# Performance work log

Hardware: AMD Instinct MI355X
Metric: run time of the kernel (lower is better)

## Reference

```python
import jax, jax.numpy as jnp
import numpy as np

B = 128
N_IN = 32      # n_inp_capsules
D_IN = 8       # dim_inp_capsules
N_OUT = 10     # n_out_capsules
D_OUT = 16     # dim_out_capsules
DIM = 12       # dim_input (spatial side)
N = N_IN * DIM * DIM  # 4608 total input capsule positions
NUM_ROUTING = 3


def setup_inputs() -> dict:
    key = jax.random.key(0)
    k1, k2 = jax.random.split(key)
    x = jax.random.normal(k1, (B, D_IN, N_IN, DIM, DIM), dtype=jnp.float32)
    weight = jax.random.normal(k2, (D_IN, D_OUT, N, N_OUT), dtype=jnp.float32)
    return {"x": x, "weight": weight}


def squash(s, axis):
    # s_sq/(1+s_sq) * s / sqrt(s_sq)  -- exactly the module's squash (no eps)
    s_sq = jnp.sum(s * s, axis=axis, keepdims=True)
    return s_sq / (1.0 + s_sq) * s / jnp.sqrt(s_sq)


def reference(x, weight):
    b_sz = x.shape[0]
    # view(B, C, -1).permute(0,2,1): (B, N, D_IN)
    u = x.reshape(b_sz, D_IN, -1).transpose(0, 2, 1)
    # u_hat[b,o,n,j] = sum_d u[b,n,d] * weight[d,o,n,j]  (replaces the double python loop)
    u_hat = jnp.einsum('bnd,donj->bonj', u, weight)  # (B, D_OUT, N, N_OUT)
    b = jnp.zeros((b_sz, 1, N, N_OUT), dtype=u_hat.dtype)
    s = None
    for _ in range(NUM_ROUTING):
        c = jax.nn.softmax(b, axis=3)                      # over output capsules
        s = squash(jnp.sum(u_hat * c, axis=2), axis=1)     # (B, D_OUT, N_OUT)
        b = b + jnp.sum(s[:, :, None, :] * u_hat, axis=1, keepdims=True)
    return s  # torch returns s.squeeze() of (B, D_OUT, 1, N_OUT) -> (B, D_OUT, N_OUT)
```

## Files before the change

kernel.cpp:

```cpp
#include <hip/hip_runtime.h>
#include <math.h>

#define NTOT 4608

typedef _Float16 f16;
typedef _Float16 f16x4 __attribute__((ext_vector_type(4)));
typedef _Float16 f16x8 __attribute__((ext_vector_type(8)));
typedef float f32x4 __attribute__((ext_vector_type(4)));

__global__ __launch_bounds__(256) void make_ut(const float* __restrict__ x, f16* __restrict__ ut) {
    const int t = blockIdx.x * 256 + threadIdx.x;
    const int b = t / NTOT, n = t - b * NTOT;
    f16x8 v;
    #pragma unroll
    for (int d = 0; d < 8; ++d)
        v[d] = (f16)x[((size_t)b * 8 + d) * NTOT + n];
    *reinterpret_cast<f16x8*>(ut + (size_t)t * 8) = v;
}

__global__ __launch_bounds__(320) void make_wt(const float* __restrict__ W, f16* __restrict__ wt) {
    __shared__ float l[2560];
    const int k = threadIdx.x;
    const int n0 = blockIdx.x * 2;
    #pragma unroll
    for (int r = 0; r < 8; ++r) {
        const int f = k + r * 320;
        const int p = f / 20, q = f - p * 20;
        l[f] = W[(size_t)p * 46080 + n0 * 10 + q];
    }
    __syncthreads();
    const int half = k / 160, rr = k - half * 160;
    const int j = rr >> 4, o = rr & 15;
    f16x8 v;
    #pragma unroll
    for (int d = 0; d < 8; ++d)
        v[d] = (f16)l[d * 320 + o * 20 + half * 10 + j];
    *reinterpret_cast<f16x8*>(wt + ((size_t)(n0 + half) * 160 + rr) * 8) = v;
}

__global__ __launch_bounds__(256) void kernelA(const f16* __restrict__ ut, const f16* __restrict__ wt,
                                               f16* __restrict__ uh, float* __restrict__ partial) {
    __shared__ float s0t[4][16][164];
    const int tid = threadIdx.x, w = tid >> 6, lane = tid & 63;
    const int col = lane & 15, qA = lane >> 4;
    const int chunk = blockIdx.x, bg = blockIdx.y, b0 = bg * 16;
    const int b = b0 + col;
    const int nstart = chunk * 32 + w * 8;

    const f16* ab = wt + ((size_t)nstart * 160 + col) * 8;
    const f16* ub = ut + ((size_t)b * NTOT + nstart) * 8;
    f16* uhw = uh + (size_t)nstart * 20480 + (size_t)(qA >> 1) * 1024 + b * 8 + (qA & 1) * 4;

    const f32x4 cz = {0.f, 0.f, 0.f, 0.f};
    f32x4 s0a[10];
    #pragma unroll
    for (int m = 0; m < 10; ++m) s0a[m] = cz;

    for (int nl = 0; nl < 8; ++nl) {
        const f16x8 bf = *reinterpret_cast<const f16x8*>(ub + nl * 8);
        #pragma unroll
        for (int m = 0; m < 10; ++m) {
            const f16x8 af = *reinterpret_cast<const f16x8*>(ab + ((size_t)nl * 160 + m * 16) * 8);
            f32x4 C = __builtin_amdgcn_mfma_f32_16x16x32_f16(af, bf, cz, 0, 0, 0);
            s0a[m] += C;
            f16x4 hv;
            hv[0] = (f16)(0.25f * C[0]); hv[1] = (f16)(0.25f * C[1]);
            hv[2] = (f16)(0.25f * C[2]); hv[3] = (f16)(0.25f * C[3]);
            *reinterpret_cast<f16x4*>(uhw + (size_t)nl * 20480 + m * 2048) = hv;
        }
    }

    #pragma unroll
    for (int m = 0; m < 10; ++m)
        *reinterpret_cast<f32x4*>(&s0t[w][col][m * 16 + qA * 4]) = s0a[m];
    __syncthreads();
    for (int r = tid; r < 2560; r += 256) {
        const int row = r / 160, slot = r - row * 160;
        float v = s0t[0][row][slot] + s0t[1][row][slot] + s0t[2][row][slot] + s0t[3][row][slot];
        partial[((size_t)chunk * 128 + b0 + row) * 160 + slot] = v;
    }
}

__global__ __launch_bounds__(256) void kernelB(const f16* __restrict__ uh, const float* __restrict__ Ar,
                                               float* __restrict__ partial) {
    __shared__ float s1t[4][16][164];
    const int tid = threadIdx.x, w = tid >> 6, lane = tid & 63;
    const int g = lane & 15, q = lane >> 4;
    const int chunk = blockIdx.x, bg = blockIdx.y;
    const int b = bg * 16 + g;
    const int nstart = chunk * 16 + w * 4;
    const bool qlow = (q < 2);

    float Af[5][8];
    #pragma unroll
    for (int s = 0; s < 5; ++s) {
        f32x4 a0 = *reinterpret_cast<const f32x4*>(Ar + (size_t)b * 160 + (4 * s + q) * 8);
        f32x4 a1 = *reinterpret_cast<const f32x4*>(Ar + (size_t)b * 160 + (4 * s + q) * 8 + 4);
        #pragma unroll
        for (int t = 0; t < 4; ++t) { Af[s][t] = a0[t]; Af[s][4 + t] = a1[t]; }
    }

    float P[5][8];
    #pragma unroll
    for (int s = 0; s < 5; ++s)
        #pragma unroll
        for (int t = 0; t < 8; ++t) P[s][t] = 0.f;

    const f16* uhb = uh + (size_t)nstart * 20480 + (size_t)q * 1024 + b * 8;

    for (int nl = 0; nl < 4; ++nl) {
        f16x8 U[5];
        #pragma unroll
        for (int s = 0; s < 5; ++s)
            U[s] = *reinterpret_cast<const f16x8*>(uhb + (size_t)nl * 20480 + s * 4096);

        float tp[5];
        #pragma unroll
        for (int s = 0; s < 5; ++s) {
            float acc = 0.f;
            #pragma unroll
            for (int t = 0; t < 8; ++t)
                acc = fmaf(Af[s][t], (float)U[s][t], acc);
            tp[s] = acc;
        }

        float tt[10];
        #pragma unroll
        for (int s = 0; s < 5; ++s) {
            float tq = tp[s] + __shfl_xor(tp[s], 16, 64);
            float tr = __shfl_xor(tq, 32, 64);
            tt[2 * s]     = qlow ? tq : tr;
            tt[2 * s + 1] = qlow ? tr : tq;
        }

        float mx = fmaxf(fmaxf(fmaxf(fmaxf(tt[0], tt[1]), fmaxf(tt[2], tt[3])),
                               fmaxf(fmaxf(tt[4], tt[5]), fmaxf(tt[6], tt[7]))),
                         fmaxf(tt[8], tt[9]));
        float c[10], sum = 0.f;
        #pragma unroll
        for (int j = 0; j < 10; ++j) { float e = __expf(tt[j] - mx); c[j] = e; sum += e; }
        const float inv = 1.0f / sum;

        #pragma unroll
        for (int s = 0; s < 5; ++s) {
            const float cm = (qlow ? c[2 * s] : c[2 * s + 1]) * inv;
            #pragma unroll
            for (int t = 0; t < 8; ++t)
                P[s][t] = fmaf(cm, (float)U[s][t], P[s][t]);
        }
    }

    #pragma unroll
    for (int s = 0; s < 5; ++s) {
        const int sg = 4 * s + q;
        f32x4 p0 = {P[s][0], P[s][1], P[s][2], P[s][3]};
        f32x4 p1 = {P[s][4], P[s][5], P[s][6], P[s][7]};
        *reinterpret_cast<f32x4*>(&s1t[w][g][sg * 8])     = p0;
        *reinterpret_cast<f32x4*>(&s1t[w][g][sg * 8 + 4]) = p1;
    }
    __syncthreads();
    for (int r = tid; r < 2560; r += 256) {
        const int row = r / 160, slot = r - row * 160;
        float v = s1t[0][row][slot] + s1t[1][row][slot] + s1t[2][row][slot] + s1t[3][row][slot];
        partial[((size_t)chunk * 128 + bg * 16 + row) * 160 + slot] = v;
    }
}

__global__ __launch_bounds__(160) void red1(const float* __restrict__ partial,
                                            float* __restrict__ p2, int nc8) {
    const int b = blockIdx.x, sl = blockIdx.y, k = threadIdx.x;
    const float* p = partial + ((size_t)sl * nc8 * 128 + b) * 160 + k;
    float acc = 0.f;
    for (int c = 0; c < nc8; ++c) acc += p[(size_t)c * 128 * 160];
    p2[((size_t)b * 8 + sl) * 160 + k] = acc;
}

template<int MODE>
__global__ __launch_bounds__(160) void phase2f(const float* __restrict__ p2,
                                               float* __restrict__ Ar, float* __restrict__ out,
                                               float sumscale) {
    const int b = blockIdx.x, k = threadIdx.x;
    __shared__ float srs[160];
    float acc = 0.f;
    #pragma unroll
    for (int sl = 0; sl < 8; ++sl) acc += p2[((size_t)b * 8 + sl) * 160 + k];
    acc *= sumscale;
    srs[k] = acc;
    __syncthreads();
    const int j = k >> 4;
    float ssq = 0.f;
    #pragma unroll
    for (int o = 0; o < 16; ++o) { float v = srs[j * 16 + o]; ssq = fmaf(v, v, ssq); }
    const float s = acc * ssq / ((1.f + ssq) * sqrtf(ssq));
    if (MODE == 0)      Ar[(size_t)b * 160 + k] = s;
    else if (MODE == 1) Ar[(size_t)b * 160 + k] += s;
    else { const int o = k & 15; out[(size_t)b * 160 + o * 10 + j] = s; }
}

extern "C" void kernel_launch(void* const* d_in, const int* in_sizes, int n_in,
                              void* d_out, int out_size, void* d_ws, size_t ws_size,
                              hipStream_t stream) {
    const float* x = (const float*)d_in[0];
    const float* W = (const float*)d_in[1];
    float* out = (float*)d_out;

    f16* ut = (f16*)d_ws;
    f16* wt = ut + (size_t)128 * NTOT * 8;
    f16* uh = wt + (size_t)NTOT * 160 * 8;
    float* Ar = (float*)(uh + (size_t)NTOT * 20 * 128 * 8);
    float* partial = Ar + 128 * 160;
    float* p2 = partial + (size_t)288 * 128 * 160;

    make_ut<<<2304, 256, 0, stream>>>(x, ut);
    make_wt<<<2304, 320, 0, stream>>>(W, wt);

    dim3 gA(144, 8), gB(288, 8), gR(128, 8);
    kernelA<<<gA, 256, 0, stream>>>(ut, wt, uh, partial);
    red1<<<gR, 160, 0, stream>>>(partial, p2, 144 / 8);
    phase2f<0><<<128, 160, 0, stream>>>(p2, Ar, out, 0.025f);

    kernelB<<<gB, 256, 0, stream>>>(uh, Ar, partial);
    red1<<<gR, 160, 0, stream>>>(partial, p2, 288 / 8);
    phase2f<1><<<128, 160, 0, stream>>>(p2, Ar, out, 1.0f);

    kernelB<<<gB, 256, 0, stream>>>(uh, Ar, partial);
    red1<<<gR, 160, 0, stream>>>(partial, p2, 288 / 8);
    phase2f<2><<<128, 160, 0, stream>>>(p2, Ar, out, 1.0f);
}
```

Measured before the change: 174.6 us.

## Fuse prep kernels, merge reduction with squash, and double kernelB work per block

Merges the two input-conversion kernels into one launch, with the block index choosing between weight transpose and input transpose. Replaces the two-stage red1+phase2f reduction with one 640-thread kernel per batch that sums partials and squashes. Makes each kernelB block cover 32 positions instead of 16, halving the partial count so it matches kernelA's layout. This cuts launch count and partial-buffer traffic, at the cost of fewer blocks in kernelB. It also adds a __syncthreads inside a branch whose condition splits a wavefront, which is risky.

```diff
diff --git a/kernel.cpp b/kernel.cpp
--- a/kernel.cpp
+++ b/kernel.cpp
@@ -8,34 +8,37 @@
 typedef _Float16 f16x8 __attribute__((ext_vector_type(8)));
 typedef float f32x4 __attribute__((ext_vector_type(4)));
 
-__global__ __launch_bounds__(256) void make_ut(const float* __restrict__ x, f16* __restrict__ ut) {
-    const int t = blockIdx.x * 256 + threadIdx.x;
-    const int b = t / NTOT, n = t - b * NTOT;
-    f16x8 v;
-    #pragma unroll
-    for (int d = 0; d < 8; ++d)
-        v[d] = (f16)x[((size_t)b * 8 + d) * NTOT + n];
-    *reinterpret_cast<f16x8*>(ut + (size_t)t * 8) = v;
-}
-
-__global__ __launch_bounds__(320) void make_wt(const float* __restrict__ W, f16* __restrict__ wt) {
+__global__ __launch_bounds__(320) void prep(const float* __restrict__ x, const float* __restrict__ W,
+                                            f16* __restrict__ ut, f16* __restrict__ wt) {
     __shared__ float l[2560];
     const int k = threadIdx.x;
-    const int n0 = blockIdx.x * 2;
-    #pragma unroll
-    for (int r = 0; r < 8; ++r) {
-        const int f = k + r * 320;
-        const int p = f / 20, q = f - p * 20;
-        l[f] = W[(size_t)p * 46080 + n0 * 10 + q];
-    }
-    __syncthreads();
-    const int half = k / 160, rr = k - half * 160;
-    const int j = rr >> 4, o = rr & 15;
-    f16x8 v;
-    #pragma unroll
-    for (int d = 0; d < 8; ++d)
-        v[d] = (f16)l[d * 320 + o * 20 + half * 10 + j];
-    *reinterpret_cast<f16x8*>(wt + ((size_t)(n0 + half) * 160 + rr) * 8) = v;
+    if (blockIdx.x < 2304) {
+        const int n0 = blockIdx.x * 2;
+        #pragma unroll
+        for (int r = 0; r < 8; ++r) {
+            const int f = k + r * 320;
+            const int p = f / 20, q = f - p * 20;
+            l[f] = W[(size_t)p * 46080 + n0 * 10 + q];
+        }
+        __syncthreads();
+        const int half = k / 160, rr = k - half * 160;
+        const int j = rr >> 4, o = rr & 15;
+        f16x8 v;
+        #pragma unroll
+        for (int d = 0; d < 8; ++d)
+            v[d] = (f16)l[d * 320 + o * 20 + half * 10 + j];
+        *reinterpret_cast<f16x8*>(wt + ((size_t)(n0 + half) * 160 + rr) * 8) = v;
+    } else {
+        const int t = (blockIdx.x - 2304) * 320 + k;
+        if (t < 128 * NTOT) {
+            const int b = t / NTOT, n = t - b * NTOT;
+            f16x8 v;
+            #pragma unroll
+            for (int d = 0; d < 8; ++d)
+                v[d] = (f16)x[((size_t)b * 8 + d) * NTOT + n];
+            *reinterpret_cast<f16x8*>(ut + (size_t)t * 8) = v;
+        }
+    }
 }
 
 __global__ __launch_bounds__(256) void kernelA(const f16* __restrict__ ut, const f16* __restrict__ wt,
@@ -88,7 +91,7 @@
     const int g = lane & 15, q = lane >> 4;
     const int chunk = blockIdx.x, bg = blockIdx.y;
     const int b = bg * 16 + g;
-    const int nstart = chunk * 16 + w * 4;
+    const int nstart = chunk * 32 + w * 8;
     const bool qlow = (q < 2);
 
     float Af[5][8];
@@ -108,7 +111,7 @@
 
     const f16* uhb = uh + (size_t)nstart * 20480 + (size_t)q * 1024 + b * 8;
 
-    for (int nl = 0; nl < 4; ++nl) {
+    for (int nl = 0; nl < 8; ++nl) {
         f16x8 U[5];
         #pragma unroll
         for (int s = 0; s < 5; ++s)
@@ -166,35 +169,34 @@
     }
 }
 
-__global__ __launch_bounds__(160) void red1(const float* __restrict__ partial,
-                                            float* __restrict__ p2, int nc8) {
-    const int b = blockIdx.x, sl = blockIdx.y, k = threadIdx.x;
-    const float* p = partial + ((size_t)sl * nc8 * 128 + b) * 160 + k;
+template<int MODE>
+__global__ __launch_bounds__(640) void reduce_squash(const float* __restrict__ partial,
+                                                     float* __restrict__ Ar, float* __restrict__ out,
+                                                     float sumscale) {
+    const int b = blockIdx.x;
+    const int k = threadIdx.x % 160;
+    const int r = threadIdx.x / 160;
+    __shared__ float red[4][160];
     float acc = 0.f;
-    for (int c = 0; c < nc8; ++c) acc += p[(size_t)c * 128 * 160];
-    p2[((size_t)b * 8 + sl) * 160 + k] = acc;
-}
-
-template<int MODE>
-__global__ __launch_bounds__(160) void phase2f(const float* __restrict__ p2,
-                                               float* __restrict__ Ar, float* __restrict__ out,
-                                               float sumscale) {
-    const int b = blockIdx.x, k = threadIdx.x;
-    __shared__ float srs[160];
-    float acc = 0.f;
-    #pragma unroll
-    for (int sl = 0; sl < 8; ++sl) acc += p2[((size_t)b * 8 + sl) * 160 + k];
-    acc *= sumscale;
-    srs[k] = acc;
+    for (int c = r; c < 144; c += 4)
+        acc += partial[((size_t)c * 128 + b) * 160 + k];
+    red[r][k] = acc;
     __syncthreads();
-    const int j = k >> 4;
-    float ssq = 0.f;
-    #pragma unroll
-    for (int o = 0; o < 16; ++o) { float v = srs[j * 16 + o]; ssq = fmaf(v, v, ssq); }
-    const float s = acc * ssq / ((1.f + ssq) * sqrtf(ssq));
-    if (MODE == 0)      Ar[(size_t)b * 160 + k] = s;
-    else if (MODE == 1) Ar[(size_t)b * 160 + k] += s;
-    else { const int o = k & 15; out[(size_t)b * 160 + o * 10 + j] = s; }
+    if (r == 0) {
+        float a = (red[0][k] + red[1][k] + red[2][k] + red[3][k]) * sumscale;
+        red[0][k] = a;
+        __syncthreads();
+        const int j = k >> 4;
+        float ssq = 0.f;
+        #pragma unroll
+        for (int o = 0; o < 16; ++o) { float v = red[0][j * 16 + o]; ssq = fmaf(v, v, ssq); }
+        const float s = a * ssq / ((1.f + ssq) * sqrtf(ssq));
+        if (MODE == 0)      Ar[(size_t)b * 160 + k] = s;
+        else if (MODE == 1) Ar[(size_t)b * 160 + k] += s;
+        else { const int o = k & 15; out[(size_t)b * 160 + o * 10 + j] = s; }
+    } else {
+        __syncthreads();
+    }
 }
 
 extern "C" void kernel_launch(void* const* d_in, const int* in_sizes, int n_in,
@@ -209,21 +211,16 @@
     f16* uh = wt + (size_t)NTOT * 160 * 8;
     float* Ar = (float*)(uh + (size_t)NTOT * 20 * 128 * 8);
     float* partial = Ar + 128 * 160;
-    float* p2 = partial + (size_t)288 * 128 * 160;
-
-    make_ut<<<2304, 256, 0, stream>>>(x, ut);
-    make_wt<<<2304, 320, 0, stream>>>(W, wt);
-
-    dim3 gA(144, 8), gB(288, 8), gR(128, 8);
+
+    prep<<<2304 + 1844, 320, 0, stream>>>(x, W, ut, wt);
+
+    dim3 gA(144, 8);
     kernelA<<<gA, 256, 0, stream>>>(ut, wt, uh, partial);
-    red1<<<gR, 160, 0, stream>>>(partial, p2, 144 / 8);
-    phase2f<0><<<128, 160, 0, stream>>>(p2, Ar, out, 0.025f);
-
-    kernelB<<<gB, 256, 0, stream>>>(uh, Ar, partial);
-    red1<<<gR, 160, 0, stream>>>(partial, p2, 288 / 8);
-    phase2f<1><<<128, 160, 0, stream>>>(p2, Ar, out, 1.0f);
-
-    kernelB<<<gB, 256, 0, stream>>>(uh, Ar, partial);
-    red1<<<gR, 160, 0, stream>>>(partial, p2, 288 / 8);
-    phase2f<2><<<128, 160, 0, stream>>>(p2, Ar, out, 1.0f);
-}
+    reduce_squash<0><<<128, 640, 0, stream>>>(partial, Ar, out, 0.025f);
+
+    kernelB<<<gA, 256, 0, stream>>>(uh, Ar, partial);
+    reduce_squash<1><<<128, 640, 0, stream>>>(partial, Ar, out, 1.0f);
+
+    kernelB<<<gA, 256, 0, stream>>>(uh, Ar, partial);
+    reduce_squash<2><<<128, 640, 0, stream>>>(partial, Ar, out, 1.0f);
+}
```

New measurement: 166.0 us. -5.0%, faster.
